# Kernel tuning notes

Measured on AMD Instinct MI355X. Metric: run time of the kernel, lower is better.

Reference implementation:

```python
import jax, jax.numpy as jnp
import numpy as np
import math

N = 8192
FIN = 256
FOUT = 256


def setup_inputs() -> dict:
    key = jax.random.key(0)
    k1, k2, k3, k4 = jax.random.split(key, 4)
    x = jax.random.normal(k1, (N, FIN), dtype=jnp.float32)
    adj = jax.random.uniform(k2, (N, N), dtype=jnp.float32)
    stdv = 1.0 / math.sqrt(FOUT)
    W = jax.random.uniform(k3, (FIN, FOUT), minval=-stdv, maxval=stdv, dtype=jnp.float32)
    b = jax.random.uniform(k4, (FOUT,), minval=-stdv, maxval=stdv, dtype=jnp.float32)
    return {"input": x, "adj": adj, "W": W, "b": b}


def reference(input, adj, W, b):
    # add self-loops, then symmetric degree normalization: D^{-1/2} A D^{-1/2}
    A = adj + jnp.eye(adj.shape[0], dtype=adj.dtype)
    D = 1.0 / jnp.sqrt(jnp.sum(A, axis=1))          # [N]
    A = A * D[:, None] * D[None, :]                  # normalized adjacency [N, N]
    support = input @ W                              # [N, FOUT]
    out = A @ support                                # aggregation (dense equiv of sparse.mm)
    return jax.nn.relu(out + b)
```

## Files before the change

kernel.cpp:

```cpp
#include <hip/hip_runtime.h>
#include <hip/hip_bf16.h>

#define NROW 8192
#define FINC 256
#define FOUTC 256
#define BM 32
#define BK 64
#define NT (NROW / BK)

typedef __attribute__((ext_vector_type(8))) short bf16x8;
typedef __attribute__((ext_vector_type(4))) float f32x4;

__device__ __forceinline__ unsigned short f2bf(float f) {
  unsigned u = __float_as_uint(f);
  u += 0x7fffu + ((u >> 16) & 1u);
  return (unsigned short)(u >> 16);
}
__device__ __forceinline__ float bf2f(unsigned short h) {
  return __uint_as_float(((unsigned)h) << 16);
}

__global__ __launch_bounds__(256) void rowsum_kernel(const float* __restrict__ adj,
                                                     float* __restrict__ D) {
  const int row = blockIdx.x * 4 + (threadIdx.x >> 6);
  const int l = threadIdx.x & 63;
  const float4* p = reinterpret_cast<const float4*>(adj + (size_t)row * NROW);
  float s0 = 0.f, s1 = 0.f, s2 = 0.f, s3 = 0.f;
#pragma unroll
  for (int i = 0; i < 8; ++i) {
    float4 a = p[l + (i * 4 + 0) * 64];
    float4 b = p[l + (i * 4 + 1) * 64];
    float4 c = p[l + (i * 4 + 2) * 64];
    float4 d = p[l + (i * 4 + 3) * 64];
    s0 += (a.x + a.y) + (a.z + a.w);
    s1 += (b.x + b.y) + (b.z + b.w);
    s2 += (c.x + c.y) + (c.z + c.w);
    s3 += (d.x + d.y) + (d.z + d.w);
  }
  float s = (s0 + s1) + (s2 + s3);
#pragma unroll
  for (int off = 32; off > 0; off >>= 1) s += __shfl_down(s, off, 64);
  if (l == 0) D[row] = 1.0f / sqrtf(s + 1.0f);
}

__global__ __launch_bounds__(256) void support_kernel(const float* __restrict__ x,
                                                      const float* __restrict__ W,
                                                      const float* __restrict__ D,
                                                      unsigned short* __restrict__ s2T) {
  __shared__ float xs[32][FINC];
  const int t = threadIdx.x;
  const int r0 = blockIdx.x * 32;
  {
    const float4* xg = reinterpret_cast<const float4*>(x + (size_t)r0 * FINC);
    float4* xl = reinterpret_cast<float4*>(&xs[0][0]);
#pragma unroll
    for (int i = 0; i < 8; ++i) xl[t + i * 256] = xg[t + i * 256];
  }
  __syncthreads();
  const int w = t >> 6, l = t & 63;
  float acc[8][4] = {};
  const float4* W4 = reinterpret_cast<const float4*>(W);
#pragma unroll 4
  for (int k = 0; k < FINC; ++k) {
    float4 wv = W4[k * 64 + l];
#pragma unroll
    for (int m = 0; m < 8; ++m) {
      float xv = xs[w * 8 + m][k];
      acc[m][0] = fmaf(xv, wv.x, acc[m][0]);
      acc[m][1] = fmaf(xv, wv.y, acc[m][1]);
      acc[m][2] = fmaf(xv, wv.z, acc[m][2]);
      acc[m][3] = fmaf(xv, wv.w, acc[m][3]);
    }
  }
#pragma unroll
  for (int m = 0; m < 8; ++m) {
    const int j = r0 + w * 8 + m;
    const float d = D[j];
    const int f0 = l * 4;
#pragma unroll
    for (int q = 0; q < 4; ++q)
      s2T[(size_t)(f0 + q) * NROW + j] = f2bf(d * acc[m][q]);
  }
}

__global__ __launch_bounds__(512) void gcn_gemm_kernel(const float* __restrict__ adj,
                                                       const unsigned short* __restrict__ s2T,
                                                       const float* __restrict__ D,
                                                       const float* __restrict__ bias,
                                                       float* __restrict__ out) {
  __shared__ __align__(16) unsigned short As[3][BM * BK];
  __shared__ __align__(16) unsigned short Bs[3][FOUTC * BK];

  const int t = threadIdx.x, wid = t >> 6, l = t & 63;
  const int bm0 = blockIdx.x * BM;

  const int ar = t >> 4;
  const unsigned awoff = (unsigned)(ar * 128 + (((t & 15) * 8) ^ ((ar & 7) << 4)));
  const float4* arow = reinterpret_cast<const float4*>(adj + (size_t)(bm0 + ar) * NROW) + (t & 15);

  const int bn = l >> 3;
  const unsigned bks = (unsigned)(((l & 7) * 16) ^ (bn << 4));

  f32x4 acc[2][2] = {};

  const unsigned swz = (unsigned)((l & 7) << 4);
  const int fr = l & 15;
  const unsigned kb = (unsigned)((l >> 4) * 16);
  const int nb = wid * 32;

  auto stageB = [&](int kt, int sl) {
#pragma unroll
    for (int i = 0; i < 4; ++i) {
      const int c = wid * 4 + i;
      const int n = c * 8 + bn;
      const unsigned short* src = s2T + (size_t)n * NROW + (size_t)kt * BK;
      __builtin_amdgcn_global_load_lds(
          (const __attribute__((address_space(1))) unsigned int*)((const char*)src + bks),
          (__attribute__((address_space(3))) unsigned int*)((char*)&Bs[sl][0] + c * 1024),
          16, 0, 0);
    }
  };
  auto writeA = [&](float4 av, int sl) {
    ushort4 ab;
    ab.x = f2bf(av.x); ab.y = f2bf(av.y); ab.z = f2bf(av.z); ab.w = f2bf(av.w);
    *reinterpret_cast<ushort4*>((char*)&As[sl][0] + awoff) = ab;
  };
  auto compute = [&](int sl) {
    const char* Ab = (const char*)&As[sl][0];
    const char* Bb = (const char*)&Bs[sl][0];
#pragma unroll
    for (int kk = 0; kk < 2; ++kk) {
      const unsigned kx = ((unsigned)(kk * 64) + kb) ^ swz;
      bf16x8 a0 = *reinterpret_cast<const bf16x8*>(Ab + fr * 128 + kx);
      bf16x8 a1 = *reinterpret_cast<const bf16x8*>(Ab + (fr + 16) * 128 + kx);
      bf16x8 b0 = *reinterpret_cast<const bf16x8*>(Bb + (nb + fr) * 128 + kx);
      bf16x8 b1 = *reinterpret_cast<const bf16x8*>(Bb + (nb + 16 + fr) * 128 + kx);
      acc[0][0] = __builtin_amdgcn_mfma_f32_16x16x32_bf16(a0, b0, acc[0][0], 0, 0, 0);
      acc[0][1] = __builtin_amdgcn_mfma_f32_16x16x32_bf16(a0, b1, acc[0][1], 0, 0, 0);
      acc[1][0] = __builtin_amdgcn_mfma_f32_16x16x32_bf16(a1, b0, acc[1][0], 0, 0, 0);
      acc[1][1] = __builtin_amdgcn_mfma_f32_16x16x32_bf16(a1, b1, acc[1][1], 0, 0, 0);
    }
  };

  float4 a0p, a1p, a2p;
  {
    float4 a0v = arow[0];
    asm volatile("" ::: "memory");
    stageB(0, 0);
    a1p = arow[16];
    asm volatile("" ::: "memory");
    stageB(1, 1);
    a2p = arow[32];
    asm volatile("s_waitcnt vmcnt(10)" ::: "memory");
    writeA(a0v, 0);
  }

#define PIPE_ITER(KT, S0, S1, S2, AW, AN)                                      \
  asm volatile("s_waitcnt vmcnt(5) lgkmcnt(0)\n\ts_barrier" ::: "memory");     \
  writeA(AW, S1);                                                              \
  stageB((KT) + 2, S2);                                                        \
  if ((KT) < NT - 3) AN = arow[((KT) + 3) * 16];                               \
  compute(S0);

#pragma unroll 1
  for (int kt = 0; kt < NT - 2; kt += 3) {
    PIPE_ITER(kt + 0, 0, 1, 2, a1p, a0p)
    PIPE_ITER(kt + 1, 1, 2, 0, a2p, a1p)
    PIPE_ITER(kt + 2, 2, 0, 1, a0p, a2p)
  }
#undef PIPE_ITER

  asm volatile("s_waitcnt vmcnt(4) lgkmcnt(0)\n\ts_barrier" ::: "memory");
  writeA(a1p, 1);
  compute(0);
  asm volatile("s_waitcnt vmcnt(0) lgkmcnt(0)\n\ts_barrier" ::: "memory");
  compute(1);

#pragma unroll
  for (int m = 0; m < 2; ++m) {
#pragma unroll
    for (int n = 0; n < 2; ++n) {
#pragma unroll
      for (int q = 0; q < 4; ++q) {
        const int i = bm0 + m * 16 + (l >> 4) * 4 + q;
        const int f = wid * 32 + n * 16 + fr;
        const float selfv = bf2f(s2T[(size_t)f * NROW + i]);
        float v = (acc[m][n][q] + selfv) * D[i] + bias[f];
        out[(size_t)i * FOUTC + f] = fmaxf(v, 0.0f);
      }
    }
  }
}

extern "C" void kernel_launch(void* const* d_in, const int* in_sizes, int n_in,
                              void* d_out, int out_size, void* d_ws, size_t ws_size,
                              hipStream_t stream) {
  const float* x   = (const float*)d_in[0];
  const float* adj = (const float*)d_in[1];
  const float* W   = (const float*)d_in[2];
  const float* b   = (const float*)d_in[3];
  float* out = (float*)d_out;

  float* D = (float*)d_ws;
  unsigned short* s2T = (unsigned short*)((char*)d_ws + NROW * sizeof(float));

  rowsum_kernel<<<NROW / 4, 256, 0, stream>>>(adj, D);
  support_kernel<<<NROW / 32, 256, 0, stream>>>(x, W, D, s2T);
  gcn_gemm_kernel<<<NROW / BM, 512, 0, stream>>>(adj, s2T, D, b, out);
}
```

Before: 201.9 us.

## Pre-convert adjacency to swizzled bf16 tiles in rowsum pass for direct LDS loads

Fuses the degree row-sum with converting adj to bf16 and writing it in a pre-swizzled tiled layout in workspace. The GEMM then streams A tiles with global_load_lds instead of loading fp32, converting in registers and storing to LDS. This adds a 134MB write plus a 134MB reread in place of the second fp32 read. A fallback keeps the old path when the workspace is too small.

```diff
diff --git a/kernel.cpp b/kernel.cpp
--- a/kernel.cpp
+++ b/kernel.cpp
@@ -20,27 +20,48 @@
   return __uint_as_float(((unsigned)h) << 16);
 }
 
-__global__ __launch_bounds__(256) void rowsum_kernel(const float* __restrict__ adj,
-                                                     float* __restrict__ D) {
-  const int row = blockIdx.x * 4 + (threadIdx.x >> 6);
-  const int l = threadIdx.x & 63;
-  const float4* p = reinterpret_cast<const float4*>(adj + (size_t)row * NROW);
-  float s0 = 0.f, s1 = 0.f, s2 = 0.f, s3 = 0.f;
-#pragma unroll
-  for (int i = 0; i < 8; ++i) {
-    float4 a = p[l + (i * 4 + 0) * 64];
-    float4 b = p[l + (i * 4 + 1) * 64];
-    float4 c = p[l + (i * 4 + 2) * 64];
-    float4 d = p[l + (i * 4 + 3) * 64];
-    s0 += (a.x + a.y) + (a.z + a.w);
-    s1 += (b.x + b.y) + (b.z + b.w);
-    s2 += (c.x + c.y) + (c.z + c.w);
-    s3 += (d.x + d.y) + (d.z + d.w);
-  }
-  float s = (s0 + s1) + (s2 + s3);
-#pragma unroll
-  for (int off = 32; off > 0; off >>= 1) s += __shfl_down(s, off, 64);
-  if (l == 0) D[row] = 1.0f / sqrtf(s + 1.0f);
+__global__ __launch_bounds__(1024) void prep_kernel(const float* __restrict__ adj,
+                                                    float* __restrict__ D,
+                                                    unsigned short* __restrict__ adjt) {
+  __shared__ unsigned short lds[32][1032];
+  const int t = threadIdx.x;
+  const int m = blockIdx.x;
+  const int r = t >> 5;
+  const int ph = t & 31;
+  const int slot = t & 511;
+  const int wt = slot >> 5;
+  const int wr = slot & 31;
+  const int jh = t >> 9;
+  float sum = 0.f;
+  const float* src0 = adj + (size_t)(m * 32 + r) * NROW + ph * 4;
+  unsigned short* dst0 = adjt + ((size_t)m * 128 + wt) * 2048 + wr * 64;
+
+  for (int c = 0; c < 8; ++c) {
+    const float* src = src0 + c * 1024;
+#pragma unroll
+    for (int j = 0; j < 8; ++j) {
+      float4 v = *reinterpret_cast<const float4*>(src + j * 128);
+      sum += (v.x + v.y) + (v.z + v.w);
+      ushort4 b;
+      b.x = f2bf(v.x); b.y = f2bf(v.y); b.z = f2bf(v.z); b.w = f2bf(v.w);
+      *reinterpret_cast<ushort4*>(&lds[r][j * 128 + ph * 4]) = b;
+    }
+    __syncthreads();
+    unsigned short* dst = dst0 + (size_t)c * 16 * 2048;
+#pragma unroll
+    for (int jj = 0; jj < 4; ++jj) {
+      const int j = jh * 4 + jj;
+      bf16x8 v = *reinterpret_cast<const bf16x8*>((const char*)&lds[wr][0] + wt * 128 + j * 16);
+      *reinterpret_cast<bf16x8*>((char*)dst + ((j * 16) ^ ((wr & 7) << 4))) = v;
+    }
+    __syncthreads();
+  }
+  sum += __shfl_xor(sum, 1, 64);
+  sum += __shfl_xor(sum, 2, 64);
+  sum += __shfl_xor(sum, 4, 64);
+  sum += __shfl_xor(sum, 8, 64);
+  sum += __shfl_xor(sum, 16, 64);
+  if (ph == 0) D[m * 32 + r] = rsqrtf(sum + 1.0f);
 }
 
 __global__ __launch_bounds__(256) void support_kernel(const float* __restrict__ x,
@@ -83,7 +104,7 @@
   }
 }
 
-__global__ __launch_bounds__(512) void gcn_gemm_kernel(const float* __restrict__ adj,
+__global__ __launch_bounds__(512) void gcn_gemm_kernel(const unsigned short* __restrict__ adjt,
                                                        const unsigned short* __restrict__ s2T,
                                                        const float* __restrict__ D,
                                                        const float* __restrict__ bias,
@@ -94,10 +115,6 @@
   const int t = threadIdx.x, wid = t >> 6, l = t & 63;
   const int bm0 = blockIdx.x * BM;
 
-  const int ar = t >> 4;
-  const unsigned awoff = (unsigned)(ar * 128 + (((t & 15) * 8) ^ ((ar & 7) << 4)));
-  const float4* arow = reinterpret_cast<const float4*>(adj + (size_t)(bm0 + ar) * NROW) + (t & 15);
-
   const int bn = l >> 3;
   const unsigned bks = (unsigned)(((l & 7) * 16) ^ (bn << 4));
 
@@ -108,7 +125,18 @@
   const unsigned kb = (unsigned)((l >> 4) * 16);
   const int nb = wid * 32;
 
-  auto stageB = [&](int kt, int sl) {
+  const unsigned short* atile0 = adjt + (size_t)blockIdx.x * 128 * 2048;
+
+  auto stage = [&](int kt, int sl) {
+    const char* tile = (const char*)(atile0 + (size_t)kt * 2048);
+#pragma unroll
+    for (int i = 0; i < 2; ++i) {
+      const int q = wid * 2 + i;
+      __builtin_amdgcn_global_load_lds(
+          (const __attribute__((address_space(1))) unsigned int*)(tile + q * 256 + l * 4),
+          (__attribute__((address_space(3))) unsigned int*)((char*)&As[sl][0] + q * 256),
+          4, 0, 0);
+    }
 #pragma unroll
     for (int i = 0; i < 4; ++i) {
       const int c = wid * 4 + i;
@@ -119,11 +147,6 @@
           (__attribute__((address_space(3))) unsigned int*)((char*)&Bs[sl][0] + c * 1024),
           16, 0, 0);
     }
-  };
-  auto writeA = [&](float4 av, int sl) {
-    ushort4 ab;
-    ab.x = f2bf(av.x); ab.y = f2bf(av.y); ab.z = f2bf(av.z); ab.w = f2bf(av.w);
-    *reinterpret_cast<ushort4*>((char*)&As[sl][0] + awoff) = ab;
   };
   auto compute = [&](int sl) {
     const char* Ab = (const char*)&As[sl][0];
@@ -142,6 +165,119 @@
     }
   };
 
+  stage(0, 0);
+  asm volatile("" ::: "memory");
+  stage(1, 1);
+
+#define PIPE_ITER(KT, S0, S2)                                                  \
+  asm volatile("s_waitcnt vmcnt(6) lgkmcnt(0)\n\ts_barrier" ::: "memory");     \
+  stage((KT) + 2, S2);                                                         \
+  compute(S0);
+
+#pragma unroll 1
+  for (int kt = 0; kt < NT - 2; kt += 3) {
+    PIPE_ITER(kt + 0, 0, 2)
+    PIPE_ITER(kt + 1, 1, 0)
+    PIPE_ITER(kt + 2, 2, 1)
+  }
+#undef PIPE_ITER
+
+  asm volatile("s_waitcnt vmcnt(6) lgkmcnt(0)\n\ts_barrier" ::: "memory");
+  compute(0);
+  asm volatile("s_waitcnt vmcnt(0) lgkmcnt(0)\n\ts_barrier" ::: "memory");
+  compute(1);
+
+#pragma unroll
+  for (int m = 0; m < 2; ++m) {
+#pragma unroll
+    for (int n = 0; n < 2; ++n) {
+#pragma unroll
+      for (int q = 0; q < 4; ++q) {
+        const int i = bm0 + m * 16 + (l >> 4) * 4 + q;
+        const int f = wid * 32 + n * 16 + fr;
+        const float selfv = bf2f(s2T[(size_t)f * NROW + i]);
+        float v = (acc[m][n][q] + selfv) * D[i] + bias[f];
+        out[(size_t)i * FOUTC + f] = fmaxf(v, 0.0f);
+      }
+    }
+  }
+}
+
+__global__ __launch_bounds__(256) void rowsum_kernel(const float* __restrict__ adj,
+                                                     float* __restrict__ D) {
+  const int row = blockIdx.x * 4 + (threadIdx.x >> 6);
+  const int l = threadIdx.x & 63;
+  const float4* p = reinterpret_cast<const float4*>(adj + (size_t)row * NROW);
+  float s0 = 0.f, s1 = 0.f, s2 = 0.f, s3 = 0.f;
+#pragma unroll
+  for (int i = 0; i < 8; ++i) {
+    float4 a = p[l + (i * 4 + 0) * 64];
+    float4 b = p[l + (i * 4 + 1) * 64];
+    float4 c = p[l + (i * 4 + 2) * 64];
+    float4 d = p[l + (i * 4 + 3) * 64];
+    s0 += (a.x + a.y) + (a.z + a.w);
+    s1 += (b.x + b.y) + (b.z + b.w);
+    s2 += (c.x + c.y) + (c.z + c.w);
+    s3 += (d.x + d.y) + (d.z + d.w);
+  }
+  float s = (s0 + s1) + (s2 + s3);
+#pragma unroll
+  for (int off = 32; off > 0; off >>= 1) s += __shfl_down(s, off, 64);
+  if (l == 0) D[row] = 1.0f / sqrtf(s + 1.0f);
+}
+
+__global__ __launch_bounds__(512) void gemm_fb(const float* __restrict__ adj,
+                                               const unsigned short* __restrict__ s2T,
+                                               const float* __restrict__ D,
+                                               const float* __restrict__ bias,
+                                               float* __restrict__ out) {
+  __shared__ __align__(16) unsigned short As[3][BM * BK];
+  __shared__ __align__(16) unsigned short Bs[3][FOUTC * BK];
+  const int t = threadIdx.x, wid = t >> 6, l = t & 63;
+  const int bm0 = blockIdx.x * BM;
+  const int ar = t >> 4;
+  const unsigned awoff = (unsigned)(ar * 128 + (((t & 15) * 8) ^ ((ar & 7) << 4)));
+  const float4* arow = reinterpret_cast<const float4*>(adj + (size_t)(bm0 + ar) * NROW) + (t & 15);
+  const int bn = l >> 3;
+  const unsigned bks = (unsigned)(((l & 7) * 16) ^ (bn << 4));
+  f32x4 acc[2][2] = {};
+  const unsigned swz = (unsigned)((l & 7) << 4);
+  const int fr = l & 15;
+  const unsigned kb = (unsigned)((l >> 4) * 16);
+  const int nb = wid * 32;
+  auto stageB = [&](int kt, int sl) {
+#pragma unroll
+    for (int i = 0; i < 4; ++i) {
+      const int c = wid * 4 + i;
+      const int n = c * 8 + bn;
+      const unsigned short* src = s2T + (size_t)n * NROW + (size_t)kt * BK;
+      __builtin_amdgcn_global_load_lds(
+          (const __attribute__((address_space(1))) unsigned int*)((const char*)src + bks),
+          (__attribute__((address_space(3))) unsigned int*)((char*)&Bs[sl][0] + c * 1024),
+          16, 0, 0);
+    }
+  };
+  auto writeA = [&](float4 av, int sl) {
+    ushort4 ab;
+    ab.x = f2bf(av.x); ab.y = f2bf(av.y); ab.z = f2bf(av.z); ab.w = f2bf(av.w);
+    *reinterpret_cast<ushort4*>((char*)&As[sl][0] + awoff) = ab;
+  };
+  auto compute = [&](int sl) {
+    const char* Ab = (const char*)&As[sl][0];
+    const char* Bb = (const char*)&Bs[sl][0];
+#pragma unroll
+    for (int kk = 0; kk < 2; ++kk) {
+      const unsigned kx = ((unsigned)(kk * 64) + kb) ^ swz;
+      bf16x8 a0 = *reinterpret_cast<const bf16x8*>(Ab + fr * 128 + kx);
+      bf16x8 a1 = *reinterpret_cast<const bf16x8*>(Ab + (fr + 16) * 128 + kx);
+      bf16x8 b0 = *reinterpret_cast<const bf16x8*>(Bb + (nb + fr) * 128 + kx);
+      bf16x8 b1 = *reinterpret_cast<const bf16x8*>(Bb + (nb + 16 + fr) * 128 + kx);
+      acc[0][0] = __builtin_amdgcn_mfma_f32_16x16x32_bf16(a0, b0, acc[0][0], 0, 0, 0);
+      acc[0][1] = __builtin_amdgcn_mfma_f32_16x16x32_bf16(a0, b1, acc[0][1], 0, 0, 0);
+      acc[1][0] = __builtin_amdgcn_mfma_f32_16x16x32_bf16(a1, b0, acc[1][0], 0, 0, 0);
+      acc[1][1] = __builtin_amdgcn_mfma_f32_16x16x32_bf16(a1, b1, acc[1][1], 0, 0, 0);
+    }
+  };
   float4 a0p, a1p, a2p;
   {
     float4 a0v = arow[0];
@@ -154,14 +290,12 @@
     asm volatile("s_waitcnt vmcnt(10)" ::: "memory");
     writeA(a0v, 0);
   }
-
 #define PIPE_ITER(KT, S0, S1, S2, AW, AN)                                      \
   asm volatile("s_waitcnt vmcnt(5) lgkmcnt(0)\n\ts_barrier" ::: "memory");     \
   writeA(AW, S1);                                                              \
   stageB((KT) + 2, S2);                                                        \
   if ((KT) < NT - 3) AN = arow[((KT) + 3) * 16];                               \
   compute(S0);
-
 #pragma unroll 1
   for (int kt = 0; kt < NT - 2; kt += 3) {
     PIPE_ITER(kt + 0, 0, 1, 2, a1p, a0p)
@@ -169,13 +303,11 @@
     PIPE_ITER(kt + 2, 2, 0, 1, a0p, a2p)
   }
 #undef PIPE_ITER
-
   asm volatile("s_waitcnt vmcnt(4) lgkmcnt(0)\n\ts_barrier" ::: "memory");
   writeA(a1p, 1);
   compute(0);
   asm volatile("s_waitcnt vmcnt(0) lgkmcnt(0)\n\ts_barrier" ::: "memory");
   compute(1);
-
 #pragma unroll
   for (int m = 0; m < 2; ++m) {
 #pragma unroll
@@ -202,9 +334,17 @@
   float* out = (float*)d_out;
 
   float* D = (float*)d_ws;
-  unsigned short* s2T = (unsigned short*)((char*)d_ws + NROW * sizeof(float));
-
-  rowsum_kernel<<<NROW / 4, 256, 0, stream>>>(adj, D);
-  support_kernel<<<NROW / 32, 256, 0, stream>>>(x, W, D, s2T);
-  gcn_gemm_kernel<<<NROW / BM, 512, 0, stream>>>(adj, s2T, D, b, out);
-}
+  unsigned short* s2T  = (unsigned short*)((char*)d_ws + 32768);
+  unsigned short* adjt = (unsigned short*)((char*)d_ws + 32768 + 4194304);
+
+  const size_t need = 32768ull + 4194304ull + (size_t)NROW * NROW * 2ull;
+  if (ws_size >= need) {
+    prep_kernel<<<NROW / 32, 1024, 0, stream>>>(adj, D, adjt);
+    support_kernel<<<NROW / 32, 256, 0, stream>>>(x, W, D, s2T);
+    gcn_gemm_kernel<<<NROW / BM, 512, 0, stream>>>(adjt, s2T, D, b, out);
+  } else {
+    rowsum_kernel<<<NROW / 4, 256, 0, stream>>>(adj, D);
+    support_kernel<<<NROW / 32, 256, 0, stream>>>(x, W, D, s2T);
+    gemm_fb<<<NROW / BM, 512, 0, stream>>>(adj, s2T, D, b, out);
+  }
+}
```

Result: slower. 216.3 us, median of 4 (+7.1%).

## Split-K the adjacency GEMM with larger row tiles and a combine kernel

Applied to the files above, without the earlier changes.

The main GEMM now uses 64-row tiles and splits the 8192-long K dimension into four chunks. Each block writes fp32 partial sums to workspace, and a new combine kernel sums the partials, adds the self-loop term from a row-major bf16 copy of support, then applies the D scaling, bias and ReLU. The goal is to halve redundant reads of the B operand per output row and to keep the block count up for occupancy. In exchange it adds 32 MB of partial-sum traffic, an extra kernel launch, and extra support writes, and it keeps the old kernel as a fallback when the workspace is too small.

```diff
diff --git a/kernel.cpp b/kernel.cpp
--- a/kernel.cpp
+++ b/kernel.cpp
@@ -4,9 +4,11 @@
 #define NROW 8192
 #define FINC 256
 #define FOUTC 256
-#define BM 32
+#define BM 64
 #define BK 64
-#define NT (NROW / BK)
+#define KSPLIT 4
+#define KLOC (NROW / KSPLIT)
+#define NTL (KLOC / BK)
 
 typedef __attribute__((ext_vector_type(8))) short bf16x8;
 typedef __attribute__((ext_vector_type(4))) float f32x4;
@@ -46,7 +48,8 @@
 __global__ __launch_bounds__(256) void support_kernel(const float* __restrict__ x,
                                                       const float* __restrict__ W,
                                                       const float* __restrict__ D,
-                                                      unsigned short* __restrict__ s2T) {
+                                                      unsigned short* __restrict__ s2T,
+                                                      unsigned short* __restrict__ s2R) {
   __shared__ float xs[32][FINC];
   const int t = threadIdx.x;
   const int r0 = blockIdx.x * 32;
@@ -77,37 +80,182 @@
     const int j = r0 + w * 8 + m;
     const float d = D[j];
     const int f0 = l * 4;
-#pragma unroll
-    for (int q = 0; q < 4; ++q)
-      s2T[(size_t)(f0 + q) * NROW + j] = f2bf(d * acc[m][q]);
+    ushort4 rv;
+    rv.x = f2bf(d * acc[m][0]);
+    rv.y = f2bf(d * acc[m][1]);
+    rv.z = f2bf(d * acc[m][2]);
+    rv.w = f2bf(d * acc[m][3]);
+    *reinterpret_cast<ushort4*>(&s2R[(size_t)j * FOUTC + f0]) = rv;
+    s2T[(size_t)(f0 + 0) * NROW + j] = rv.x;
+    s2T[(size_t)(f0 + 1) * NROW + j] = rv.y;
+    s2T[(size_t)(f0 + 2) * NROW + j] = rv.z;
+    s2T[(size_t)(f0 + 3) * NROW + j] = rv.w;
   }
 }
 
 __global__ __launch_bounds__(512) void gcn_gemm_kernel(const float* __restrict__ adj,
                                                        const unsigned short* __restrict__ s2T,
-                                                       const float* __restrict__ D,
-                                                       const float* __restrict__ bias,
-                                                       float* __restrict__ out) {
-  __shared__ __align__(16) unsigned short As[3][BM * BK];
+                                                       float* __restrict__ part) {
+  __shared__ __align__(16) unsigned short As[2][BM * BK];
+  __shared__ __align__(16) unsigned short Bs[2][FOUTC * BK];
+
+  const int t = threadIdx.x, wid = t >> 6, l = t & 63;
+  const int bid = blockIdx.x;
+  const int m = bid >> 2, ks = bid & 3;
+  const int bm0 = m * BM;
+  const size_t k0 = (size_t)ks * KLOC;
+
+  const int ar = t >> 3, ac = t & 7;
+  const float4* arow = reinterpret_cast<const float4*>(adj + (size_t)(bm0 + ar) * NROW + k0) + ac;
+  const unsigned awoff0 = (unsigned)(ar * 128 + ((ac * 8) ^ ((ar & 7) << 4)));
+  const unsigned awoff1 = (unsigned)(ar * 128 + ((ac * 8 + 64) ^ ((ar & 7) << 4)));
+
+  const int bn = l >> 3;
+  const unsigned bks = (unsigned)(((l & 7) * 16) ^ (bn << 4));
+
+  f32x4 acc[2][4] = {};
+
+  const int wm = wid >> 2, wn = wid & 3;
+  const int am0 = wm * 32, nb0 = wn * 64;
+  const unsigned swz = (unsigned)((l & 7) << 4);
+  const int fr = l & 15;
+  const unsigned kb = (unsigned)((l >> 4) * 16);
+
+  auto stageB = [&](int kt, int sl) {
+#pragma unroll
+    for (int i = 0; i < 4; ++i) {
+      const int c = wid * 4 + i;
+      const int n = c * 8 + bn;
+      const unsigned short* src = s2T + (size_t)n * NROW + k0 + (size_t)kt * BK;
+      __builtin_amdgcn_global_load_lds(
+          (const __attribute__((address_space(1))) unsigned int*)((const char*)src + bks),
+          (__attribute__((address_space(3))) unsigned int*)((char*)&Bs[sl][0] + c * 1024),
+          16, 0, 0);
+    }
+  };
+  auto writeA = [&](float4 v0, float4 v1, int sl) {
+    ushort4 u0, u1;
+    u0.x = f2bf(v0.x); u0.y = f2bf(v0.y); u0.z = f2bf(v0.z); u0.w = f2bf(v0.w);
+    u1.x = f2bf(v1.x); u1.y = f2bf(v1.y); u1.z = f2bf(v1.z); u1.w = f2bf(v1.w);
+    *reinterpret_cast<ushort4*>((char*)&As[sl][0] + awoff0) = u0;
+    *reinterpret_cast<ushort4*>((char*)&As[sl][0] + awoff1) = u1;
+  };
+  auto compute = [&](int sl) {
+    const char* Ab = (const char*)&As[sl][0];
+    const char* Bb = (const char*)&Bs[sl][0];
+#pragma unroll
+    for (int kk = 0; kk < 2; ++kk) {
+      const unsigned kx = ((unsigned)(kk * 64) + kb) ^ swz;
+      bf16x8 a0 = *reinterpret_cast<const bf16x8*>(Ab + (am0 + fr) * 128 + kx);
+      bf16x8 a1 = *reinterpret_cast<const bf16x8*>(Ab + (am0 + 16 + fr) * 128 + kx);
+      bf16x8 b0 = *reinterpret_cast<const bf16x8*>(Bb + (nb0 + fr) * 128 + kx);
+      bf16x8 b1 = *reinterpret_cast<const bf16x8*>(Bb + (nb0 + 16 + fr) * 128 + kx);
+      bf16x8 b2 = *reinterpret_cast<const bf16x8*>(Bb + (nb0 + 32 + fr) * 128 + kx);
+      bf16x8 b3 = *reinterpret_cast<const bf16x8*>(Bb + (nb0 + 48 + fr) * 128 + kx);
+      acc[0][0] = __builtin_amdgcn_mfma_f32_16x16x32_bf16(a0, b0, acc[0][0], 0, 0, 0);
+      acc[0][1] = __builtin_amdgcn_mfma_f32_16x16x32_bf16(a0, b1, acc[0][1], 0, 0, 0);
+      acc[0][2] = __builtin_amdgcn_mfma_f32_16x16x32_bf16(a0, b2, acc[0][2], 0, 0, 0);
+      acc[0][3] = __builtin_amdgcn_mfma_f32_16x16x32_bf16(a0, b3, acc[0][3], 0, 0, 0);
+      acc[1][0] = __builtin_amdgcn_mfma_f32_16x16x32_bf16(a1, b0, acc[1][0], 0, 0, 0);
+      acc[1][1] = __builtin_amdgcn_mfma_f32_16x16x32_bf16(a1, b1, acc[1][1], 0, 0, 0);
+      acc[1][2] = __builtin_amdgcn_mfma_f32_16x16x32_bf16(a1, b2, acc[1][2], 0, 0, 0);
+      acc[1][3] = __builtin_amdgcn_mfma_f32_16x16x32_bf16(a1, b3, acc[1][3], 0, 0, 0);
+    }
+  };
+
+  float4 aR0_0, aR0_1, aR1_0, aR1_1;
+  {
+    float4 v0 = arow[0], v1 = arow[8];
+    asm volatile("s_waitcnt vmcnt(0)" ::: "memory");
+    writeA(v0, v1, 0);
+    stageB(0, 0);
+    asm volatile("" ::: "memory");
+    aR1_0 = arow[16]; aR1_1 = arow[24];
+  }
+
+#define GITER(T, SC, SN, AW0, AW1, AN0, AN1)                                   \
+  asm volatile("s_waitcnt vmcnt(2) lgkmcnt(0)\n\ts_barrier" ::: "memory");     \
+  stageB((T) + 1, SN);                                                         \
+  asm volatile("" ::: "memory");                                               \
+  AN0 = arow[((T) + 2) * 16]; AN1 = arow[((T) + 2) * 16 + 8];                  \
+  compute(SC);                                                                 \
+  asm volatile("s_waitcnt vmcnt(6)" ::: "memory");                             \
+  writeA(AW0, AW1, SN);
+
+#pragma unroll 1
+  for (int tt = 0; tt < NTL - 2; tt += 2) {
+    GITER(tt + 0, 0, 1, aR1_0, aR1_1, aR0_0, aR0_1)
+    GITER(tt + 1, 1, 0, aR0_0, aR0_1, aR1_0, aR1_1)
+  }
+#undef GITER
+  asm volatile("s_waitcnt vmcnt(2) lgkmcnt(0)\n\ts_barrier" ::: "memory");
+  stageB(NTL - 1, 1);
+  compute(0);
+  asm volatile("s_waitcnt vmcnt(4)" ::: "memory");
+  writeA(aR1_0, aR1_1, 1);
+  asm volatile("s_waitcnt vmcnt(0) lgkmcnt(0)\n\ts_barrier" ::: "memory");
+  compute(1);
+
+  float* pout = part + (size_t)ks * NROW * FOUTC;
+#pragma unroll
+  for (int mm = 0; mm < 2; ++mm) {
+#pragma unroll
+    for (int n = 0; n < 4; ++n) {
+#pragma unroll
+      for (int q = 0; q < 4; ++q) {
+        const int i = bm0 + am0 + mm * 16 + (l >> 4) * 4 + q;
+        const int f = nb0 + n * 16 + fr;
+        pout[(size_t)i * FOUTC + f] = acc[mm][n][q];
+      }
+    }
+  }
+}
+
+__global__ __launch_bounds__(256) void combine_kernel(const float* __restrict__ part,
+                                                      const unsigned short* __restrict__ s2R,
+                                                      const float* __restrict__ D,
+                                                      const float* __restrict__ bias,
+                                                      float* __restrict__ out) {
+  const int idx = blockIdx.x * 256 + threadIdx.x;
+  const int i = idx >> 6;
+  const int f0 = (idx & 63) * 4;
+  const size_t off = (size_t)i * FOUTC + f0;
+  const size_t stride = (size_t)NROW * FOUTC;
+  float4 p0 = *reinterpret_cast<const float4*>(part + off);
+  float4 p1 = *reinterpret_cast<const float4*>(part + stride + off);
+  float4 p2 = *reinterpret_cast<const float4*>(part + 2 * stride + off);
+  float4 p3 = *reinterpret_cast<const float4*>(part + 3 * stride + off);
+  ushort4 sv = *reinterpret_cast<const ushort4*>(s2R + off);
+  float di = D[i];
+  float4 bv = *reinterpret_cast<const float4*>(bias + f0);
+  float4 o;
+  o.x = fmaxf((p0.x + p1.x + p2.x + p3.x + bf2f(sv.x)) * di + bv.x, 0.f);
+  o.y = fmaxf((p0.y + p1.y + p2.y + p3.y + bf2f(sv.y)) * di + bv.y, 0.f);
+  o.z = fmaxf((p0.z + p1.z + p2.z + p3.z + bf2f(sv.z)) * di + bv.z, 0.f);
+  o.w = fmaxf((p0.w + p1.w + p2.w + p3.w + bf2f(sv.w)) * di + bv.w, 0.f);
+  *reinterpret_cast<float4*>(out + off) = o;
+}
+
+__global__ __launch_bounds__(512) void gemm_fb(const float* __restrict__ adj,
+                                               const unsigned short* __restrict__ s2T,
+                                               const float* __restrict__ D,
+                                               const float* __restrict__ bias,
+                                               float* __restrict__ out) {
+  __shared__ __align__(16) unsigned short As[3][32 * BK];
   __shared__ __align__(16) unsigned short Bs[3][FOUTC * BK];
-
   const int t = threadIdx.x, wid = t >> 6, l = t & 63;
-  const int bm0 = blockIdx.x * BM;
-
+  const int bm0 = blockIdx.x * 32;
   const int ar = t >> 4;
   const unsigned awoff = (unsigned)(ar * 128 + (((t & 15) * 8) ^ ((ar & 7) << 4)));
   const float4* arow = reinterpret_cast<const float4*>(adj + (size_t)(bm0 + ar) * NROW) + (t & 15);
-
   const int bn = l >> 3;
   const unsigned bks = (unsigned)(((l & 7) * 16) ^ (bn << 4));
-
   f32x4 acc[2][2] = {};
-
   const unsigned swz = (unsigned)((l & 7) << 4);
   const int fr = l & 15;
   const unsigned kb = (unsigned)((l >> 4) * 16);
   const int nb = wid * 32;
-
+  const int NTF = NROW / BK;
   auto stageB = [&](int kt, int sl) {
 #pragma unroll
     for (int i = 0; i < 4; ++i) {
@@ -141,7 +289,6 @@
       acc[1][1] = __builtin_amdgcn_mfma_f32_16x16x32_bf16(a1, b1, acc[1][1], 0, 0, 0);
     }
   };
-
   float4 a0p, a1p, a2p;
   {
     float4 a0v = arow[0];
@@ -154,28 +301,24 @@
     asm volatile("s_waitcnt vmcnt(10)" ::: "memory");
     writeA(a0v, 0);
   }
-
 #define PIPE_ITER(KT, S0, S1, S2, AW, AN)                                      \
   asm volatile("s_waitcnt vmcnt(5) lgkmcnt(0)\n\ts_barrier" ::: "memory");     \
   writeA(AW, S1);                                                              \
   stageB((KT) + 2, S2);                                                        \
-  if ((KT) < NT - 3) AN = arow[((KT) + 3) * 16];                               \
+  if ((KT) < NTF - 3) AN = arow[((KT) + 3) * 16];                              \
   compute(S0);
-
 #pragma unroll 1
-  for (int kt = 0; kt < NT - 2; kt += 3) {
+  for (int kt = 0; kt < NTF - 2; kt += 3) {
     PIPE_ITER(kt + 0, 0, 1, 2, a1p, a0p)
     PIPE_ITER(kt + 1, 1, 2, 0, a2p, a1p)
     PIPE_ITER(kt + 2, 2, 0, 1, a0p, a2p)
   }
 #undef PIPE_ITER
-
   asm volatile("s_waitcnt vmcnt(4) lgkmcnt(0)\n\ts_barrier" ::: "memory");
   writeA(a1p, 1);
   compute(0);
   asm volatile("s_waitcnt vmcnt(0) lgkmcnt(0)\n\ts_barrier" ::: "memory");
   compute(1);
-
 #pragma unroll
   for (int m = 0; m < 2; ++m) {
 #pragma unroll
@@ -201,10 +344,19 @@
   const float* b   = (const float*)d_in[3];
   float* out = (float*)d_out;
 
-  float* D = (float*)d_ws;
-  unsigned short* s2T = (unsigned short*)((char*)d_ws + NROW * sizeof(float));
-
+  char* wsb = (char*)d_ws;
+  float* D            = (float*)wsb;
+  unsigned short* s2T = (unsigned short*)(wsb + 32768);
+  unsigned short* s2R = (unsigned short*)(wsb + 32768 + (1u << 22));
+  float* part         = (float*)(wsb + 32768 + (2u << 22));
+
+  const size_t need = 32768ull + (2ull << 22) + (size_t)KSPLIT * NROW * FOUTC * 4ull;
   rowsum_kernel<<<NROW / 4, 256, 0, stream>>>(adj, D);
-  support_kernel<<<NROW / 32, 256, 0, stream>>>(x, W, D, s2T);
-  gcn_gemm_kernel<<<NROW / BM, 512, 0, stream>>>(adj, s2T, D, b, out);
-}
+  support_kernel<<<NROW / 32, 256, 0, stream>>>(x, W, D, s2T, s2R);
+  if (ws_size >= need) {
+    gcn_gemm_kernel<<<(NROW / BM) * KSPLIT, 512, 0, stream>>>(adj, s2T, part);
+    combine_kernel<<<NROW * FOUTC / 1024, 256, 0, stream>>>(part, s2R, D, b, out);
+  } else {
+    gemm_fb<<<NROW / 32, 512, 0, stream>>>(adj, s2T, D, b, out);
+  }
+}
```

New measurement: 163.2 us. 1.24x faster.
